# Optimization experiments

Measured on AMD Instinct MI355X. Metric: run time of the kernel, lower is better.

## Reference

```python
import jax, jax.numpy as jnp
import numpy as np

# ---- static config (matches init_kwargs) ----
DIM = 96
H = W = D = 28
WS = 7            # window size
SS = 3            # shift size
NH = 4            # num heads
HD = DIM // NH    # head dim
SCALE = HD ** -0.5
NWIN_TOK = WS ** 3  # 343 tokens per window
HIDDEN = int(DIM * 4.0)
RPB_SIZE = (2 * WS - 1) ** 3


def _relative_position_index(ws):
    # faithful to source: rel[...,0] *= 2*ws-1 ; rel[...,1] *= 2*ws-1
    coords = np.stack(np.meshgrid(np.arange(ws), np.arange(ws), np.arange(ws), indexing='ij'))
    flat = coords.reshape(3, -1)                      # (3, N)
    rel = flat[:, :, None] - flat[:, None, :]         # (3, N, N)
    rel = rel.transpose(1, 2, 0).astype(np.int64)     # (N, N, 3)
    rel += ws - 1
    rel[:, :, 0] *= 2 * ws - 1
    rel[:, :, 1] *= 2 * ws - 1
    return rel.sum(-1)                                # (N, N)


def _attn_mask(Hh, Ww, Dd, ws, ss):
    img = np.zeros((1, Hh, Ww, Dd, 1), np.float32)
    cnt = 0
    sl = (slice(0, -ws), slice(-ws, -ss), slice(-ss, None))
    for a in sl:
        for b in sl:
            for c in sl:
                img[:, a, b, c, :] = cnt
                cnt += 1
    x = img.reshape(1, Hh // ws, ws, Ww // ws, ws, Dd // ws, ws, 1)
    mw = x.transpose(0, 1, 3, 5, 2, 4, 6, 7).reshape(-1, ws ** 3)  # (nW, N)
    am = mw[:, None, :] - mw[:, :, None]                           # (nW, N, N)
    return np.where(am != 0, -100.0, 0.0).astype(np.float32)


RPI = jnp.asarray(_relative_position_index(WS))          # (N, N) int
ATTN_MASK = jnp.asarray(_attn_mask(H, W, D, WS, SS))     # (nW, N, N)


def _ln(x, w, b, eps=1e-5):
    mu = x.mean(-1, keepdims=True)
    xc = x - mu
    var = (xc * xc).mean(-1, keepdims=True)
    return xc * jax.lax.rsqrt(var + eps) * w + b


def _window_partition(x):
    # x: (B, H, W, D, C) -> (B*nW, N, C)
    B, _, _, _, C = x.shape
    x = x.reshape(B, H // WS, WS, W // WS, WS, D // WS, WS, C)
    return x.transpose(0, 1, 3, 5, 2, 4, 6, 7).reshape(-1, NWIN_TOK, C)


def _window_reverse(wins, B):
    C = wins.shape[-1]
    x = wins.reshape(B, H // WS, W // WS, D // WS, WS, WS, WS, C)
    return x.transpose(0, 1, 4, 2, 5, 3, 6, 7).reshape(B, H, W, D, C)


def setup_inputs() -> dict:
    key = jax.random.key(0)
    ks = jax.random.split(key, 16)
    p = lambda k, shape, s: (jax.random.normal(k, shape, jnp.float32) * s)
    return {
        'x': jax.random.normal(ks[0], (4, H * W * D, DIM), jnp.float32),
        'norm1_w': jnp.ones((DIM,), jnp.float32),
        'norm1_b': jnp.zeros((DIM,), jnp.float32),
        'qkv_w': p(ks[1], (DIM, 3 * DIM), 0.02),   # (in, out)
        'qkv_b': jnp.zeros((3 * DIM,), jnp.float32),
        'rpb_table': p(ks[2], (RPB_SIZE, NH), 0.02),
        'proj_w': p(ks[3], (DIM, DIM), 0.02),
        'proj_b': jnp.zeros((DIM,), jnp.float32),
        'norm2_w': jnp.ones((DIM,), jnp.float32),
        'norm2_b': jnp.zeros((DIM,), jnp.float32),
        'fc1_w': p(ks[4], (DIM, HIDDEN), 0.02),
        'fc1_b': jnp.zeros((HIDDEN,), jnp.float32),
        'fc2_w': p(ks[5], (HIDDEN, DIM), 0.02),
        'fc2_b': jnp.zeros((DIM,), jnp.float32),
    }


def reference(x, norm1_w, norm1_b, qkv_w, qkv_b, rpb_table, proj_w, proj_b,
              norm2_w, norm2_b, fc1_w, fc1_b, fc2_w, fc2_b):
    B, L, C = x.shape
    shortcut = x

    xn = _ln(x, norm1_w, norm1_b).reshape(B, H, W, D, C)
    # cyclic shift (SW-MSA)
    xs = jnp.roll(xn, (-SS, -SS, -SS), axis=(1, 2, 3))
    xw = _window_partition(xs)                        # (B_, N, C)
    B_ = xw.shape[0]
    Nn = NWIN_TOK

    qkv = (xw @ qkv_w + qkv_b).reshape(B_, Nn, 3, NH, HD).transpose(2, 0, 3, 1, 4)
    q, k, v = qkv[0], qkv[1], qkv[2]                  # (B_, h, N, hd)
    attn = jnp.einsum('bhnd,bhmd->bhnm', q * SCALE, k)

    # relative position bias gather: (N*N,) -> (N, N, h) -> (h, N, N)
    rpb = rpb_table[RPI.reshape(-1)].reshape(Nn, Nn, NH).transpose(2, 0, 1)
    attn = attn + rpb[None]

    nW = ATTN_MASK.shape[0]
    attn = attn.reshape(B, nW, NH, Nn, Nn) + ATTN_MASK[None, :, None]
    attn = jax.nn.softmax(attn.reshape(B_, NH, Nn, Nn), axis=-1)

    out = jnp.einsum('bhnm,bhmd->bhnd', attn, v).transpose(0, 2, 1, 3).reshape(B_, Nn, C)
    out = out @ proj_w + proj_b

    xr = _window_reverse(out, B)
    xr = jnp.roll(xr, (SS, SS, SS), axis=(1, 2, 3)).reshape(B, L, C)

    x = shortcut + xr                                  # drop_path = 0 (eval)
    y = _ln(x, norm2_w, norm2_b)
    y = jax.nn.gelu(y @ fc1_w + fc1_b, approximate=False)
    return x + (y @ fc2_w + fc2_b)
```

## Files before the change

kernel.cpp:

```cpp
#include <hip/hip_runtime.h>

#define NTOK 343
#define NP   352
#define SCALE 0.2041241452319315f
#define LOG2E 1.44269504088896340736f
#define VSTR 360
#define PSTR 40

typedef __attribute__((ext_vector_type(8))) short bf16x8;
typedef __attribute__((ext_vector_type(4))) float f32x4;

__device__ __forceinline__ unsigned short f2bf(float f){
  unsigned u = __builtin_bit_cast(unsigned, f);
  u += 0x7fffu + ((u >> 16) & 1u);
  return (unsigned short)(u >> 16);
}
__device__ __forceinline__ float bflo(unsigned u){ return __builtin_bit_cast(float, u << 16); }
__device__ __forceinline__ float bfhi(unsigned u){ return __builtin_bit_cast(float, u & 0xffff0000u); }
__device__ __forceinline__ unsigned pk2(float a, float b){
  unsigned ua = __builtin_bit_cast(unsigned, a) + 0x8000u;
  unsigned ub = __builtin_bit_cast(unsigned, b) + 0x8000u;
  return __builtin_amdgcn_perm(ub, ua, 0x07060302u);
}
__device__ __forceinline__ unsigned pkrn(float a, float b){
  return (unsigned)f2bf(a) | ((unsigned)f2bf(b) << 16);
}
__device__ __forceinline__ float gelu_fast(float v){
  float u = v * v;
  float m = v * fmaf(0.044715f, u, 1.0f);
  float t = __builtin_amdgcn_exp2f(m * 2.30211422f);
  float r = __builtin_amdgcn_rcpf(t + 1.0f);
  return fmaf(-v, r, v);
}
__device__ __forceinline__ int region(int g){ return (g < 21) ? 0 : ((g < 25) ? 1 : 2); }

__global__ __launch_bounds__(256) void k_rpb(const float* __restrict__ tab, unsigned short* __restrict__ rpbH){
  const int bid = blockIdx.x;
  const int qt = bid % 22, t2 = bid / 22, kp = t2 % 11, h = t2 / 11;
  for (int e = threadIdx.x; e < 512; e += 256){
    int lane = e >> 3, slot = e & 7;
    int kth = slot >> 2, reg = slot & 3;
    int n = lane & 15, qd = lane >> 4;
    int i = qt * 16 + n;
    int j = (2 * kp + kth) * 16 + qd * 4 + reg;
    float v;
    if (j >= NTOK) v = -1e30f;
    else if (i >= NTOK) v = 0.f;
    else {
      int r1 = i / 49, rm = i - r1 * 49, r2 = rm / 7, r3 = rm - r2 * 7;
      int j1 = j / 49, jm = j - j1 * 49, j2 = jm / 7, j3 = jm - j2 * 7;
      int idx = 13 * ((r1 - j1) + (r2 - j2) + 12) + (r3 - j3) + 6;
      v = tab[idx * 4 + h] * LOG2E;
    }
    rpbH[(size_t)bid * 512 + e] = f2bf(v);
  }
}

__global__ __launch_bounds__(256) void k_wprep1(const float* __restrict__ qw, unsigned short* __restrict__ wQ){
  int p = blockIdx.x * 256 + threadIdx.x;
  int e = p & 7, m = (p >> 3) & 15, cell = p >> 7;
  int mt = cell / 12, kq = cell - mt * 12;
  wQ[p] = f2bf(qw[(kq * 8 + e) * 288 + mt * 16 + m]);
}

__global__ __launch_bounds__(256) void k_wprep2(
    const float* __restrict__ pw, const float* __restrict__ w1g, const float* __restrict__ w2g,
    unsigned short* __restrict__ w1F, unsigned short* __restrict__ w2F, unsigned short* __restrict__ wP)
{
  int p = blockIdx.x * 256 + threadIdx.x;
  if (p < 36864){
    int e = p & 7, m = (p >> 3) & 15, cell = p >> 7;
    int mt = cell / 12, q = cell - mt * 12;
    w1F[p] = f2bf(w1g[(q * 8 + e) * 384 + mt * 16 + m]);
  } else if (p < 73728){
    int p2 = p - 36864;
    int e = p2 & 7, m = (p2 >> 3) & 15, cell = p2 >> 7;
    int omt = cell / 48, q = cell - omt * 48;
    w2F[p2] = f2bf(w2g[(q * 8 + e) * 96 + omt * 16 + m]);
  } else {
    int p3 = p - 73728;
    int e = p3 & 7, m = (p3 >> 3) & 15, cell = p3 >> 7;
    int mt = cell / 12, kq = cell - mt * 12;
    wP[p3] = f2bf(pw[(kq * 8 + e) * 96 + mt * 16 + m]);
  }
}

__global__ __launch_bounds__(256, 4) void k_qkv(
    const float* __restrict__ x, const float* __restrict__ n1w, const float* __restrict__ n1b,
    const unsigned short* __restrict__ wQ, const float* __restrict__ qb,
    unsigned short* __restrict__ qS, unsigned short* __restrict__ kS, unsigned short* __restrict__ vT)
{
  __shared__ __align__(16) unsigned short xnF[11 * 12 * 16 * 8];
  const int blk = blockIdx.x, w = blk >> 1, half = blk & 1;
  const int b = w >> 6, wl = w & 63;
  const int wx = wl >> 4, wy = (wl >> 2) & 3, wz = wl & 3;
  const int tid = threadIdx.x, lane = tid & 63, wv = tid >> 6;

  const float g1 = n1w[lane], h1 = n1b[lane];
  const float g2 = (lane < 32) ? n1w[64 + lane] : 0.f;
  const float h2 = (lane < 32) ? n1b[64 + lane] : 0.f;
  for (int r = wv; r < 176; r += 4){
    int tl = half * 176 + r;
    int tok = (tl < NTOK) ? tl : NTOK - 1;
    int tx = tok / 49, rm = tok - tx * 49, ty = rm / 7, tz = rm - ty * 7;
    int sx = (wx * 7 + tx + 3) % 28, sy = (wy * 7 + ty + 3) % 28, sz = (wz * 7 + tz + 3) % 28;
    const float* xr = x + ((size_t)b * 21952 + ((sx * 28 + sy) * 28 + sz)) * 96;
    float v1 = xr[lane];
    float v2 = (lane < 32) ? xr[64 + lane] : 0.f;
    float s = v1 + v2, sq = v1 * v1 + v2 * v2;
    #pragma unroll
    for (int off = 32; off; off >>= 1){ s += __shfl_xor(s, off); sq += __shfl_xor(sq, off); }
    float mu = s * (1.f / 96.f);
    float rs = rsqrtf(sq * (1.f / 96.f) - mu * mu + 1e-5f);
    int nt = r >> 4, n = r & 15;
    xnF[((nt * 12 + (lane >> 3)) * 16 + n) * 8 + (lane & 7)] = f2bf((v1 - mu) * rs * g1 + h1);
    if (lane < 32){
      int cc = 64 + lane;
      xnF[((nt * 12 + (cc >> 3)) * 16 + n) * 8 + (cc & 7)] = f2bf((v2 - mu) * rs * g2 + h2);
    }
  }
  __syncthreads();

  const int ln = lane & 15, qd = lane >> 4;
  bf16x8 bfr[3][3];
  int nts[3], toks[3];
  #pragma unroll
  for (int t = 0; t < 3; t++){
    int nt = wv + 4 * t;
    nts[t] = (nt < 11) ? nt : -1;
    int ntc = (nt < 11) ? nt : 0;
    toks[t] = half * 176 + ntc * 16 + ln;
    #pragma unroll
    for (int ks = 0; ks < 3; ks++)
      bfr[t][ks] = *(const bf16x8*)(xnF + ((ntc * 12 + ks * 4 + qd) * 16 + ln) * 8);
  }
  for (int mt = 0; mt < 18; mt++){
    bf16x8 afr[3];
    #pragma unroll
    for (int ks = 0; ks < 3; ks++)
      afr[ks] = *(const bf16x8*)(wQ + ((mt * 12 + ks * 4 + qd) * 16 + ln) * 8);
    f32x4 acc[3];
    #pragma unroll
    for (int t = 0; t < 3; t++){ acc[t][0] = 0.f; acc[t][1] = 0.f; acc[t][2] = 0.f; acc[t][3] = 0.f; }
    #pragma unroll
    for (int ks = 0; ks < 3; ks++)
      #pragma unroll
      for (int t = 0; t < 3; t++)
        acc[t] = __builtin_amdgcn_mfma_f32_16x16x32_bf16(afr[ks], bfr[t][ks], acc[t], 0, 0, 0);
    const int o0 = mt * 16 + 4 * qd;
    float4 bv = *(const float4*)(qb + o0);
    const int s3 = o0 / 96, om = o0 - s3 * 96, hh = om / 24, dd = om - hh * 24;
    if (s3 < 2){
      const float sc = (s3 == 0) ? (SCALE * LOG2E) : 1.f;
      unsigned short* hb = ((s3 == 0) ? qS : kS) + ((size_t)(w * 4 + hh)) * 8232 + dd;
      #pragma unroll
      for (int t = 0; t < 3; t++){
        if (nts[t] < 0 || toks[t] >= NTOK) continue;
        uint2 st;
        st.x = pkrn((acc[t][0] + bv.x) * sc, (acc[t][1] + bv.y) * sc);
        st.y = pkrn((acc[t][2] + bv.z) * sc, (acc[t][3] + bv.w) * sc);
        *(uint2*)(hb + (size_t)toks[t] * 24) = st;
      }
    } else {
      unsigned short* hb = vT + ((size_t)(w * 4 + hh)) * 8256 + (size_t)dd * 344;
      #pragma unroll
      for (int t = 0; t < 3; t++){
        if (nts[t] < 0 || toks[t] >= NTOK) continue;
        hb[0 * 344 + toks[t]] = f2bf(acc[t][0] + bv.x);
        hb[1 * 344 + toks[t]] = f2bf(acc[t][1] + bv.y);
        hb[2 * 344 + toks[t]] = f2bf(acc[t][2] + bv.z);
        hb[3 * 344 + toks[t]] = f2bf(acc[t][3] + bv.w);
      }
    }
  }
}

__global__ __launch_bounds__(256, 4) void k_attn(
    const unsigned short* __restrict__ qS, const unsigned short* __restrict__ kS,
    const unsigned short* __restrict__ vT, const unsigned short* __restrict__ rpbH,
    unsigned short* __restrict__ aO)
{
  __shared__ __align__(16) unsigned short VTsh[25 * VSTR];
  __shared__ __align__(16) unsigned short Psh[4 * 16 * PSTR];
  __shared__ __align__(8) unsigned char lab8[NP];

  const int blk = blockIdx.x, w = blk >> 2, h = blk & 3;
  const int tid = threadIdx.x, lane = tid & 63, wv = tid >> 6;
  const int ln = lane & 15, qd = lane >> 4;

  {
    const unsigned* vg = (const unsigned*)(vT + (size_t)blk * 8256);
    unsigned* vd = (unsigned*)VTsh;
    for (int i = tid; i < 4128; i += 256){
      int d = i / 172, c = i - d * 172;
      vd[d * 180 + c] = vg[i];
    }
    for (int i = tid; i < 192; i += 256){
      int d = i >> 3, c = i & 7;
      vd[d * 180 + 172 + c] = 0u;
    }
    for (int i = tid; i < 180; i += 256) vd[24 * 180 + i] = 0x3f803f80u;
    const int wl = w & 63, wx = wl >> 4, wy = (wl >> 2) & 3, wz = wl & 3;
    for (int n = tid; n < NP; n += 256){
      int tx = n / 49, nm = n - tx * 49, ty = nm / 7, tz = nm - ty * 7;
      lab8[n] = (n < NTOK) ? (unsigned char)(region(wx*7+tx)*9 + region(wy*7+ty)*3 + region(wz*7+tz)) : (unsigned char)0;
    }
  }
  __syncthreads();

  bf16x8 qf[6];
  int labQ[6], qts[6];
  #pragma unroll
  for (int t = 0; t < 6; t++){
    int qtr = wv + 4 * t;
    bool val = qtr < 22;
    qts[t] = val ? qtr : -1;
    int qt = val ? qtr : 0;
    int query = qt * 16 + ln;
    uint4 qv = *(const uint4*)(qS + (size_t)blk * 8232 + (size_t)query * 24 + qd * 8);
    if (qd == 3){ qv.x = 0; qv.y = 0; qv.z = 0; qv.w = 0; }
    qf[t] = __builtin_bit_cast(bf16x8, qv);
    labQ[t] = lab8[qt * 16 + ln];
  }

  f32x4 accO[6][2];
  #pragma unroll
  for (int t = 0; t < 6; t++)
    #pragma unroll
    for (int d2 = 0; d2 < 2; d2++){ accO[t][d2][0]=0.f; accO[t][d2][1]=0.f; accO[t][d2][2]=0.f; accO[t][d2][3]=0.f; }

  const unsigned short* biasBase = rpbH + (size_t)h * (11 * 22 * 512);
  unsigned short* pb = Psh + wv * 16 * PSTR + ln * PSTR;
  const unsigned short* pr = Psh + wv * 16 * PSTR + ln * PSTR + qd * 8;
  const int vrow1 = (ln < 8) ? (16 + ln) : 24;
  const size_t kbase = (size_t)blk * 8232;

  for (int kp = 0; kp < 11; kp++){
    uint4 kv0 = *(const uint4*)(kS + kbase + (size_t)(kp * 32 + ln) * 24 + qd * 8);
    uint4 kv1 = *(const uint4*)(kS + kbase + (size_t)(kp * 32 + 16 + ln) * 24 + qd * 8);
    bf16x8 kf0 = __builtin_bit_cast(bf16x8, kv0);
    bf16x8 kf1 = __builtin_bit_cast(bf16x8, kv1);
    bf16x8 vf0 = *(const bf16x8*)(VTsh + ln * VSTR + kp * 32 + qd * 8);
    bf16x8 vf1 = *(const bf16x8*)(VTsh + vrow1 * VSTR + kp * 32 + qd * 8);
    const unsigned* l32 = (const unsigned*)lab8;
    unsigned la = l32[kp * 8 + qd];
    unsigned lb = l32[kp * 8 + 4 + qd];
    int kl0[4], kl1[4];
    #pragma unroll
    for (int r = 0; r < 4; r++){ kl0[r] = (la >> (8 * r)) & 255; kl1[r] = (lb >> (8 * r)) & 255; }

    #pragma unroll
    for (int t = 0; t < 6; t++){
      if (qts[t] < 0) continue;
      const int qt = qts[t];
      uint4 bv = *(const uint4*)(biasBase + (((size_t)kp * 22 + qt) * 64 + lane) * 8);
      f32x4 C0, C1;
      C0[0] = bflo(bv.x); C0[1] = bfhi(bv.x); C0[2] = bflo(bv.y); C0[3] = bfhi(bv.y);
      C1[0] = bflo(bv.z); C1[1] = bfhi(bv.z); C1[2] = bflo(bv.w); C1[3] = bfhi(bv.w);
      f32x4 s0 = __builtin_amdgcn_mfma_f32_16x16x32_bf16(kf0, qf[t], C0, 0, 0, 0);
      f32x4 s1 = __builtin_amdgcn_mfma_f32_16x16x32_bf16(kf1, qf[t], C1, 0, 0, 0);
      const int lq = labQ[t];
      float e0[4], e1[4];
      #pragma unroll
      for (int r = 0; r < 4; r++){
        float ev = __builtin_amdgcn_exp2f(s0[r]);
        e0[r] = (kl0[r] == lq) ? ev : 0.f;
      }
      #pragma unroll
      for (int r = 0; r < 4; r++){
        float ev = __builtin_amdgcn_exp2f(s1[r]);
        e1[r] = (kl1[r] == lq) ? ev : 0.f;
      }
      uint2 w0; w0.x = pk2(e0[0], e0[1]); w0.y = pk2(e0[2], e0[3]);
      uint2 w1; w1.x = pk2(e1[0], e1[1]); w1.y = pk2(e1[2], e1[3]);
      *(uint2*)(pb + 4 * qd)      = w0;
      *(uint2*)(pb + 16 + 4 * qd) = w1;
      bf16x8 pf = *(const bf16x8*)pr;
      accO[t][0] = __builtin_amdgcn_mfma_f32_16x16x32_bf16(vf0, pf, accO[t][0], 0, 0, 0);
      accO[t][1] = __builtin_amdgcn_mfma_f32_16x16x32_bf16(vf1, pf, accO[t][1], 0, 0, 0);
    }
  }

  #pragma unroll
  for (int t = 0; t < 6; t++){
    if (qts[t] < 0) continue;
    float ss = __shfl(accO[t][1][0], 32 + ln);
    float inv = 1.f / ss;
    int query = qts[t] * 16 + ln;
    if (query < NTOK){
      unsigned short* dst = aO + (size_t)w * 32928 + (size_t)query * 96 + h * 24;
      uint2 o0;
      o0.x = pkrn(accO[t][0][0] * inv, accO[t][0][1] * inv);
      o0.y = pkrn(accO[t][0][2] * inv, accO[t][0][3] * inv);
      *(uint2*)(dst + 4 * qd) = o0;
      if (qd < 2){
        uint2 o1;
        o1.x = pkrn(accO[t][1][0] * inv, accO[t][1][1] * inv);
        o1.y = pkrn(accO[t][1][2] * inv, accO[t][1][3] * inv);
        *(uint2*)(dst + 16 + 4 * qd) = o1;
      }
    }
  }
}

__global__ __launch_bounds__(256, 4) void k_proj(
    const unsigned short* __restrict__ aO, const unsigned short* __restrict__ wP,
    const float* __restrict__ pb, const float* __restrict__ x, float* __restrict__ out)
{
  __shared__ __align__(16) unsigned short aF[11 * 12 * 16 * 8];
  const int blk = blockIdx.x, w = blk >> 1, half = blk & 1;
  const int b = w >> 6, wl = w & 63;
  const int wx = wl >> 4, wy = (wl >> 2) & 3, wz = wl & 3;
  const int tid = threadIdx.x, lane = tid & 63, wv = tid >> 6;

  for (int i = tid; i < 2112; i += 256){
    int r = i / 12, kq = i - r * 12;
    int tl = half * 176 + r;
    uint4 v;
    if (tl < NTOK) v = *(const uint4*)(aO + (size_t)w * 32928 + (size_t)tl * 96 + kq * 8);
    else { v.x = 0u; v.y = 0u; v.z = 0u; v.w = 0u; }
    int nt = r >> 4, n = r & 15;
    *(uint4*)(aF + ((nt * 12 + kq) * 16 + n) * 8) = v;
  }
  __syncthreads();

  const int ln = lane & 15, qd = lane >> 4;
  bf16x8 bfr[3][3];
  int nts[3]; size_t oi[3]; bool tv[3];
  #pragma unroll
  for (int t = 0; t < 3; t++){
    int nt = wv + 4 * t;
    nts[t] = (nt < 11) ? nt : -1;
    int ntc = (nt < 11) ? nt : 0;
    int tok = half * 176 + ntc * 16 + ln;
    tv[t] = (nts[t] >= 0) && (tok < NTOK);
    int tk = (tok < NTOK) ? tok : 0;
    int tx = tk / 49, rm = tk - tx * 49, ty = rm / 7, tz = rm - ty * 7;
    int sx = (wx * 7 + tx + 3) % 28, sy = (wy * 7 + ty + 3) % 28, sz = (wz * 7 + tz + 3) % 28;
    oi[t] = ((size_t)b * 21952 + ((sx * 28 + sy) * 28 + sz)) * 96;
    #pragma unroll
    for (int ks = 0; ks < 3; ks++)
      bfr[t][ks] = *(const bf16x8*)(aF + ((ntc * 12 + ks * 4 + qd) * 16 + ln) * 8);
  }
  for (int mt = 0; mt < 6; mt++){
    bf16x8 afr[3];
    #pragma unroll
    for (int ks = 0; ks < 3; ks++)
      afr[ks] = *(const bf16x8*)(wP + ((mt * 12 + ks * 4 + qd) * 16 + ln) * 8);
    f32x4 acc[3];
    #pragma unroll
    for (int t = 0; t < 3; t++){ acc[t][0] = 0.f; acc[t][1] = 0.f; acc[t][2] = 0.f; acc[t][3] = 0.f; }
    #pragma unroll
    for (int ks = 0; ks < 3; ks++)
      #pragma unroll
      for (int t = 0; t < 3; t++)
        acc[t] = __builtin_amdgcn_mfma_f32_16x16x32_bf16(afr[ks], bfr[t][ks], acc[t], 0, 0, 0);
    const int c0 = mt * 16 + 4 * qd;
    float4 bv = *(const float4*)(pb + c0);
    #pragma unroll
    for (int t = 0; t < 3; t++){
      if (!tv[t]) continue;
      float4 cur = *(const float4*)(x + oi[t] + c0);
      float4 o;
      o.x = acc[t][0] + bv.x + cur.x;
      o.y = acc[t][1] + bv.y + cur.y;
      o.z = acc[t][2] + bv.z + cur.z;
      o.w = acc[t][3] + bv.w + cur.w;
      *(float4*)(out + oi[t] + c0) = o;
    }
  }
}

__global__ __launch_bounds__(512, 2) void k_mlp(
    float* __restrict__ io, const float* __restrict__ n2w, const float* __restrict__ n2b,
    const unsigned short* __restrict__ w1F, const float* __restrict__ b1g,
    const unsigned short* __restrict__ w2F, const float* __restrict__ b2g)
{
  __shared__ __align__(16) unsigned short xnF[4 * 12 * 16 * 8];
  __shared__ __align__(16) unsigned short hF[4 * 48 * 16 * 8];
  const int tid = threadIdx.x, lane = tid & 63, wv = tid >> 6;
  const size_t row0 = (size_t)blockIdx.x * 64;

  const float g1 = n2w[lane], c1 = n2b[lane];
  const float g2 = (lane < 32) ? n2w[64 + lane] : 0.f;
  const float c2 = (lane < 32) ? n2b[64 + lane] : 0.f;
  for (int r = wv; r < 64; r += 8){
    const float* xr = io + (row0 + r) * 96;
    float v1 = xr[lane], v2 = (lane < 32) ? xr[64 + lane] : 0.f;
    float s = v1 + v2, sq = v1 * v1 + v2 * v2;
    #pragma unroll
    for (int off = 32; off; off >>= 1){ s += __shfl_xor(s, off); sq += __shfl_xor(sq, off); }
    float mu = s * (1.f / 96.f);
    float rs = rsqrtf(sq * (1.f / 96.f) - mu * mu + 1e-5f);
    int nt = r >> 4, n = r & 15;
    xnF[((nt * 12 + (lane >> 3)) * 16 + n) * 8 + (lane & 7)] = f2bf((v1 - mu) * rs * g1 + c1);
    if (lane < 32){
      int cc = 64 + lane;
      xnF[((nt * 12 + (cc >> 3)) * 16 + n) * 8 + (cc & 7)] = f2bf((v2 - mu) * rs * g2 + c2);
    }
  }
  __syncthreads();

  const int h = lane & 15, q = lane >> 4;
  const int nt = wv & 3, mh = wv >> 2;

  f32x4 acc[12];
  #pragma unroll
  for (int mt = 0; mt < 12; mt++){
    int o0 = (mh * 12 + mt) * 16 + 4 * q;
    float4 bv = *(const float4*)(b1g + o0);
    acc[mt][0] = bv.x; acc[mt][1] = bv.y; acc[mt][2] = bv.z; acc[mt][3] = bv.w;
  }
  for (int ks = 0; ks < 3; ks++){
    bf16x8 bfr = *(const bf16x8*)(xnF + ((nt * 12 + ks * 4 + q) * 16 + h) * 8);
    #pragma unroll
    for (int mt = 0; mt < 12; mt++){
      bf16x8 afr = *(const bf16x8*)(w1F + (((mh * 12 + mt) * 12 + ks * 4 + q) * 16 + h) * 8);
      acc[mt] = __builtin_amdgcn_mfma_f32_16x16x32_bf16(afr, bfr, acc[mt], 0, 0, 0);
    }
  }
  #pragma unroll
  for (int mt = 0; mt < 12; mt++){
    int o0 = (mh * 12 + mt) * 16 + 4 * q;
    float g0 = gelu_fast(acc[mt][0]), g1v = gelu_fast(acc[mt][1]);
    float g2v = gelu_fast(acc[mt][2]), g3 = gelu_fast(acc[mt][3]);
    unsigned short* d = hF + ((nt * 48 + (o0 >> 3)) * 16 + h) * 8 + (o0 & 7);
    uint2 pkv; pkv.x = pk2(g0, g1v); pkv.y = pk2(g2v, g3);
    *(uint2*)d = pkv;
  }
  __syncthreads();

  f32x4 acc2[3];
  #pragma unroll
  for (int mt = 0; mt < 3; mt++){
    int o0 = (mh * 3 + mt) * 16 + 4 * q;
    float4 bv = *(const float4*)(b2g + o0);
    acc2[mt][0] = bv.x; acc2[mt][1] = bv.y; acc2[mt][2] = bv.z; acc2[mt][3] = bv.w;
  }
  for (int ks = 0; ks < 12; ks++){
    bf16x8 bfr = *(const bf16x8*)(hF + ((nt * 48 + ks * 4 + q) * 16 + h) * 8);
    #pragma unroll
    for (int mt = 0; mt < 3; mt++){
      bf16x8 afr = *(const bf16x8*)(w2F + (((mh * 3 + mt) * 48 + ks * 4 + q) * 16 + h) * 8);
      acc2[mt] = __builtin_amdgcn_mfma_f32_16x16x32_bf16(afr, bfr, acc2[mt], 0, 0, 0);
    }
  }
  float* orow = io + (row0 + nt * 16 + h) * 96;
  #pragma unroll
  for (int mt = 0; mt < 3; mt++){
    int o0 = (mh * 3 + mt) * 16 + 4 * q;
    float4 cur = *(const float4*)(orow + o0);
    cur.x += acc2[mt][0]; cur.y += acc2[mt][1]; cur.z += acc2[mt][2]; cur.w += acc2[mt][3];
    *(float4*)(orow + o0) = cur;
  }
}

extern "C" void kernel_launch(void* const* d_in, const int* in_sizes, int n_in,
                              void* d_out, int out_size, void* d_ws, size_t ws_size,
                              hipStream_t stream)
{
  const float* x      = (const float*)d_in[0];
  const float* n1w    = (const float*)d_in[1];
  const float* n1b    = (const float*)d_in[2];
  const float* qkvw   = (const float*)d_in[3];
  const float* qkvb   = (const float*)d_in[4];
  const float* rpbtab = (const float*)d_in[5];
  const float* projw  = (const float*)d_in[6];
  const float* projb  = (const float*)d_in[7];
  const float* n2w    = (const float*)d_in[8];
  const float* n2b    = (const float*)d_in[9];
  const float* fc1w   = (const float*)d_in[10];
  const float* fc1b   = (const float*)d_in[11];
  const float* fc2w   = (const float*)d_in[12];
  const float* fc2b   = (const float*)d_in[13];
  float* out = (float*)d_out;

  unsigned short* qS   = (unsigned short*)d_ws;
  unsigned short* kS   = qS + 8429568;
  unsigned short* vT   = kS + 8429568;
  unsigned short* aO   = vT + 8454144;
  unsigned short* rpbH = aO + 8429568;
  unsigned short* wQ  = aO;
  unsigned short* w1F = qS;
  unsigned short* w2F = qS + 36864;
  unsigned short* wP  = qS + 73728;

  k_rpb   <<<dim3(968),  dim3(256), 0, stream>>>(rpbtab, rpbH);
  k_wprep1<<<dim3(108),  dim3(256), 0, stream>>>(qkvw, wQ);
  k_qkv   <<<dim3(512),  dim3(256), 0, stream>>>(x, n1w, n1b, wQ, qkvb, qS, kS, vT);
  k_attn  <<<dim3(1024), dim3(256), 0, stream>>>(qS, kS, vT, rpbH, aO);
  k_wprep2<<<dim3(324),  dim3(256), 0, stream>>>(projw, fc1w, fc2w, w1F, w2F, wP);
  k_proj  <<<dim3(512),  dim3(256), 0, stream>>>(aO, wP, projb, x, out);
  k_mlp   <<<dim3(1372), dim3(512), 0, stream>>>(out, n2w, n2b, w1F, fc1b, w2F, fc2b);
}
```

Measured before the change: 281.3 us.

## Split fused MLP into FC1 and FC2 kernels with register and LDS weight reuse

Replaces the single fused MLP kernel with two kernels. The first applies LayerNorm and FC1+GELU over 256 rows per block, keeping FC1 weight fragments in registers across 16 row tiles, and writes the bf16 hidden activations to global workspace. The second stages the whole FC2 weight matrix (144KB) in LDS and computes 4 row tiles per wave, adding the result into the residual output. This cuts repeated global weight-fragment loads, at the cost of a round trip of the hidden activations through global memory, an extra launch, large LDS use limiting occupancy, and only 343 blocks per kernel.

```diff
diff --git a/kernel.cpp b/kernel.cpp
--- a/kernel.cpp
+++ b/kernel.cpp
@@ -371,20 +371,19 @@
   }
 }
 
-__global__ __launch_bounds__(512, 2) void k_mlp(
-    float* __restrict__ io, const float* __restrict__ n2w, const float* __restrict__ n2b,
+__global__ __launch_bounds__(512, 4) void k_fc1(
+    const float* __restrict__ io, const float* __restrict__ n2w, const float* __restrict__ n2b,
     const unsigned short* __restrict__ w1F, const float* __restrict__ b1g,
-    const unsigned short* __restrict__ w2F, const float* __restrict__ b2g)
-{
-  __shared__ __align__(16) unsigned short xnF[4 * 12 * 16 * 8];
-  __shared__ __align__(16) unsigned short hF[4 * 48 * 16 * 8];
+    unsigned short* __restrict__ hid)
+{
+  __shared__ __align__(16) unsigned short xnF[16 * 12 * 16 * 8];
   const int tid = threadIdx.x, lane = tid & 63, wv = tid >> 6;
-  const size_t row0 = (size_t)blockIdx.x * 64;
+  const size_t row0 = (size_t)blockIdx.x * 256;
 
   const float g1 = n2w[lane], c1 = n2b[lane];
   const float g2 = (lane < 32) ? n2w[64 + lane] : 0.f;
   const float c2 = (lane < 32) ? n2b[64 + lane] : 0.f;
-  for (int r = wv; r < 64; r += 8){
+  for (int r = wv; r < 256; r += 8){
     const float* xr = io + (row0 + r) * 96;
     float v1 = xr[lane], v2 = (lane < 32) ? xr[64 + lane] : 0.f;
     float s = v1 + v2, sq = v1 * v1 + v2 * v2;
@@ -402,56 +401,100 @@
   __syncthreads();
 
   const int h = lane & 15, q = lane >> 4;
-  const int nt = wv & 3, mh = wv >> 2;
-
-  f32x4 acc[12];
-  #pragma unroll
-  for (int mt = 0; mt < 12; mt++){
-    int o0 = (mh * 12 + mt) * 16 + 4 * q;
-    float4 bv = *(const float4*)(b1g + o0);
-    acc[mt][0] = bv.x; acc[mt][1] = bv.y; acc[mt][2] = bv.z; acc[mt][3] = bv.w;
-  }
-  for (int ks = 0; ks < 3; ks++){
-    bf16x8 bfr = *(const bf16x8*)(xnF + ((nt * 12 + ks * 4 + q) * 16 + h) * 8);
-    #pragma unroll
-    for (int mt = 0; mt < 12; mt++){
-      bf16x8 afr = *(const bf16x8*)(w1F + (((mh * 12 + mt) * 12 + ks * 4 + q) * 16 + h) * 8);
-      acc[mt] = __builtin_amdgcn_mfma_f32_16x16x32_bf16(afr, bfr, acc[mt], 0, 0, 0);
-    }
-  }
-  #pragma unroll
-  for (int mt = 0; mt < 12; mt++){
-    int o0 = (mh * 12 + mt) * 16 + 4 * q;
-    float g0 = gelu_fast(acc[mt][0]), g1v = gelu_fast(acc[mt][1]);
-    float g2v = gelu_fast(acc[mt][2]), g3 = gelu_fast(acc[mt][3]);
-    unsigned short* d = hF + ((nt * 48 + (o0 >> 3)) * 16 + h) * 8 + (o0 & 7);
-    uint2 pkv; pkv.x = pk2(g0, g1v); pkv.y = pk2(g2v, g3);
-    *(uint2*)d = pkv;
+  bf16x8 afr[3][3];
+  float4 bv[3];
+  #pragma unroll
+  for (int i = 0; i < 3; i++){
+    int mt = wv * 3 + i;
+    #pragma unroll
+    for (int ks = 0; ks < 3; ks++)
+      afr[i][ks] = *(const bf16x8*)(w1F + ((mt * 12 + ks * 4 + q) * 16 + h) * 8);
+    bv[i] = *(const float4*)(b1g + mt * 16 + 4 * q);
+  }
+  for (int nt = 0; nt < 16; nt++){
+    bf16x8 bfr[3];
+    #pragma unroll
+    for (int ks = 0; ks < 3; ks++)
+      bfr[ks] = *(const bf16x8*)(xnF + ((nt * 12 + ks * 4 + q) * 16 + h) * 8);
+    f32x4 acc[3];
+    #pragma unroll
+    for (int i = 0; i < 3; i++){
+      acc[i][0] = bv[i].x; acc[i][1] = bv[i].y; acc[i][2] = bv[i].z; acc[i][3] = bv[i].w;
+    }
+    #pragma unroll
+    for (int ks = 0; ks < 3; ks++)
+      #pragma unroll
+      for (int i = 0; i < 3; i++)
+        acc[i] = __builtin_amdgcn_mfma_f32_16x16x32_bf16(afr[i][ks], bfr[ks], acc[i], 0, 0, 0);
+    const size_t NT = (size_t)blockIdx.x * 16 + nt;
+    #pragma unroll
+    for (int i = 0; i < 3; i++){
+      int o0 = (wv * 3 + i) * 16 + 4 * q;
+      float g0 = gelu_fast(acc[i][0]), g1v = gelu_fast(acc[i][1]);
+      float g2v = gelu_fast(acc[i][2]), g3 = gelu_fast(acc[i][3]);
+      unsigned short* d = hid + ((NT * 48 + (o0 >> 3)) * 16 + h) * 8 + (o0 & 7);
+      uint2 pkv; pkv.x = pk2(g0, g1v); pkv.y = pk2(g2v, g3);
+      *(uint2*)d = pkv;
+    }
+  }
+}
+
+__global__ __launch_bounds__(512, 4) void k_fc2(
+    float* __restrict__ io, const unsigned short* __restrict__ hid,
+    const unsigned short* __restrict__ w2F, const float* __restrict__ b2g)
+{
+  __shared__ __align__(16) unsigned short w2sh[73728];
+  const int tid = threadIdx.x, lane = tid & 63, wv = tid >> 6;
+  {
+    const uint2* src = (const uint2*)w2F;
+    uint2* dst = (uint2*)w2sh;
+    for (int i = tid; i < 18432; i += 512) dst[i] = src[i];
   }
   __syncthreads();
 
-  f32x4 acc2[3];
-  #pragma unroll
-  for (int mt = 0; mt < 3; mt++){
-    int o0 = (mh * 3 + mt) * 16 + 4 * q;
-    float4 bv = *(const float4*)(b2g + o0);
-    acc2[mt][0] = bv.x; acc2[mt][1] = bv.y; acc2[mt][2] = bv.z; acc2[mt][3] = bv.w;
-  }
+  const int h = lane & 15, q = lane >> 4;
+  const int mh = wv >> 2, ntl = wv & 3;
+  float4 bv[3];
+  #pragma unroll
+  for (int i = 0; i < 3; i++) bv[i] = *(const float4*)(b2g + (mh * 3 + i) * 16 + 4 * q);
+
+  f32x4 acc[3][4];
+  #pragma unroll
+  for (int i = 0; i < 3; i++)
+    #pragma unroll
+    for (int j = 0; j < 4; j++){
+      acc[i][j][0] = bv[i].x; acc[i][j][1] = bv[i].y; acc[i][j][2] = bv[i].z; acc[i][j][3] = bv[i].w;
+    }
+
+  const size_t NT0 = (size_t)blockIdx.x * 16;
   for (int ks = 0; ks < 12; ks++){
-    bf16x8 bfr = *(const bf16x8*)(hF + ((nt * 48 + ks * 4 + q) * 16 + h) * 8);
-    #pragma unroll
-    for (int mt = 0; mt < 3; mt++){
-      bf16x8 afr = *(const bf16x8*)(w2F + (((mh * 3 + mt) * 48 + ks * 4 + q) * 16 + h) * 8);
-      acc2[mt] = __builtin_amdgcn_mfma_f32_16x16x32_bf16(afr, bfr, acc2[mt], 0, 0, 0);
-    }
-  }
-  float* orow = io + (row0 + nt * 16 + h) * 96;
-  #pragma unroll
-  for (int mt = 0; mt < 3; mt++){
-    int o0 = (mh * 3 + mt) * 16 + 4 * q;
-    float4 cur = *(const float4*)(orow + o0);
-    cur.x += acc2[mt][0]; cur.y += acc2[mt][1]; cur.z += acc2[mt][2]; cur.w += acc2[mt][3];
-    *(float4*)(orow + o0) = cur;
+    bf16x8 afr[3];
+    #pragma unroll
+    for (int i = 0; i < 3; i++)
+      afr[i] = *(const bf16x8*)(w2sh + (((mh * 3 + i) * 48 + ks * 4 + q) * 16 + h) * 8);
+    bf16x8 bfr[4];
+    #pragma unroll
+    for (int j = 0; j < 4; j++){
+      size_t NT = NT0 + ntl + 4 * j;
+      bfr[j] = *(const bf16x8*)(hid + ((NT * 48 + ks * 4 + q) * 16 + h) * 8);
+    }
+    #pragma unroll
+    for (int j = 0; j < 4; j++)
+      #pragma unroll
+      for (int i = 0; i < 3; i++)
+        acc[i][j] = __builtin_amdgcn_mfma_f32_16x16x32_bf16(afr[i], bfr[j], acc[i][j], 0, 0, 0);
+  }
+
+  #pragma unroll
+  for (int j = 0; j < 4; j++){
+    float* orow = io + ((NT0 + ntl + 4 * j) * 16 + h) * 96;
+    #pragma unroll
+    for (int i = 0; i < 3; i++){
+      int c0 = (mh * 3 + i) * 16 + 4 * q;
+      float4 cur = *(const float4*)(orow + c0);
+      cur.x += acc[i][j][0]; cur.y += acc[i][j][1]; cur.z += acc[i][j][2]; cur.w += acc[i][j][3];
+      *(float4*)(orow + c0) = cur;
+    }
   }
 }
 
@@ -484,6 +527,7 @@
   unsigned short* w1F = qS;
   unsigned short* w2F = qS + 36864;
   unsigned short* wP  = qS + 73728;
+  unsigned short* hid = qS + 82944;
 
   k_rpb   <<<dim3(968),  dim3(256), 0, stream>>>(rpbtab, rpbH);
   k_wprep1<<<dim3(108),  dim3(256), 0, stream>>>(qkvw, wQ);
@@ -491,5 +535,6 @@
   k_attn  <<<dim3(1024), dim3(256), 0, stream>>>(qS, kS, vT, rpbH, aO);
   k_wprep2<<<dim3(324),  dim3(256), 0, stream>>>(projw, fc1w, fc2w, w1F, w2F, wP);
   k_proj  <<<dim3(512),  dim3(256), 0, stream>>>(aO, wP, projb, x, out);
-  k_mlp   <<<dim3(1372), dim3(512), 0, stream>>>(out, n2w, n2b, w1F, fc1b, w2F, fc2b);
-}
+  k_fc1   <<<dim3(343),  dim3(512), 0, stream>>>(out, n2w, n2b, w1F, fc1b, hid);
+  k_fc2   <<<dim3(343),  dim3(512), 0, stream>>>(out, hid, w2F, fc2b);
+}
```

Result: slower. 308.8 us (+9.8%).
